# Kernel optimization log

Measured on AMD Instinct MI355X. Metric: run time of the kernel, lower is better.

The kernel has to match this reference:

```python
import jax, jax.numpy as jnp
import numpy as np

N_DENSE = 13
N_SPARSE = 26
EMBED_DIM = 16
VOCAB = 100000
N_PAIRS = N_SPARSE * (N_SPARSE - 1) // 2  # 325
I_IDX, J_IDX = np.triu_indices(N_SPARSE, k=1)  # loop order i<j matches tf code


def setup_inputs() -> dict:
    key = jax.random.key(0)
    ks = jax.random.split(key, 8)
    B = 2048
    inputs = jax.random.randint(ks[0], (B, N_DENSE + N_SPARSE), 0, VOCAB, dtype=jnp.int32)
    tables = jax.random.normal(ks[1], (N_SPARSE, VOCAB, EMBED_DIM), dtype=jnp.float32) * 0.05
    # Attention_layer: Dense(n_pairs, relu) applied along k, then Dense(1)
    w1 = jax.random.normal(ks[2], (EMBED_DIM, N_PAIRS), dtype=jnp.float32) * 0.05
    b1 = jnp.zeros((N_PAIRS,), dtype=jnp.float32)
    w2 = jax.random.normal(ks[3], (N_PAIRS, 1), dtype=jnp.float32) * 0.05
    b2 = jnp.zeros((1,), dtype=jnp.float32)
    wout = jax.random.normal(ks[4], (EMBED_DIM, 1), dtype=jnp.float32) * 0.05
    bout = jnp.zeros((1,), dtype=jnp.float32)
    return {"inputs": inputs, "tables": tables, "w1": w1, "b1": b1,
            "w2": w2, "b2": b2, "wout": wout, "bout": bout}


def reference(inputs, tables, w1, b1, w2, b2, wout, bout):
    sparse = inputs[:, N_DENSE:]                                  # [B, 26]
    # multi-table embedding lookup: tables[f, sparse[:, f]] for each field
    embed = tables[jnp.arange(N_SPARSE)[None, :], sparse]         # [B, 26, 16]
    # pairwise element-wise products (upper triangle, i<j)
    pairs = embed[:, I_IDX] * embed[:, J_IDX]                     # [B, 325, 16]
    # attention MLP (note: softmax over last axis of size 1 -> all ones, as in tf code)
    x = jax.nn.relu(pairs @ w1 + b1)                              # [B, 325, 325]
    score = x @ w2 + b2                                           # [B, 325, 1]
    a = jax.nn.softmax(score, axis=-1)                            # [B, 325, 1] (ones)
    pooled = jnp.matmul(jnp.swapaxes(a, 1, 2), pairs)             # [B, 1, 16]
    pooled = pooled.reshape(-1, EMBED_DIM)                        # [B, 16]
    return jax.nn.sigmoid(pooled @ wout + bout)                   # [B, 1]
```

## Files before the change

### kernel.cpp

```cpp
#include <hip/hip_runtime.h>
#include <math.h>

#define N_DENSE   13
#define N_SPARSE  26
#define EMBED_DIM 16
#define VOCAB     100000
#define NB        2048
#define NCOL      (N_DENSE + N_SPARSE)

__global__ __launch_bounds__(256) void afm_kernel(
    const int*   __restrict__ inputs,
    const float* __restrict__ tables,
    const float* __restrict__ wout,
    const float* __restrict__ bout,
    float*       __restrict__ out)
{
    int tid = blockIdx.x * blockDim.x + threadIdx.x;
    int b    = tid >> 5;
    int t    = tid & 31;
    int e    = t & 15;
    int half = t >> 4;
    if (b >= NB) return;

    const int* idx = inputs + b * NCOL + N_DENSE;

    float sum = 0.f, sumsq = 0.f;
    #pragma unroll
    for (int k = 0; k < 13; ++k) {
        int f = half * 13 + k;
        int ix = idx[f];
        float v = tables[((size_t)f * VOCAB + (size_t)ix) * EMBED_DIM + e];
        sum   += v;
        sumsq += v * v;
    }

    sum   += __shfl_xor(sum,   16, 32);
    sumsq += __shfl_xor(sumsq, 16, 32);

    float pooled  = 0.5f * (sum * sum - sumsq);
    float partial = pooled * wout[e];

    #pragma unroll
    for (int off = 8; off >= 1; off >>= 1)
        partial += __shfl_xor(partial, off, 16);

    if (t == 0) {
        float s = partial + bout[0];
        out[b] = 1.0f / (1.0f + expf(-s));
    }
}

extern "C" void kernel_launch(void* const* d_in, const int* in_sizes, int n_in,
                              void* d_out, int out_size, void* d_ws, size_t ws_size,
                              hipStream_t stream) {
    const int*   inputs = (const int*)  d_in[0];
    const float* tables = (const float*)d_in[1];
    const float* wout   = (const float*)d_in[6];
    const float* bout   = (const float*)d_in[7];
    float* out = (float*)d_out;

    const int threads_per_sample = 32;
    const int block = 256;
    const int total = NB * threads_per_sample;
    const int grid  = (total + block - 1) / block;

    afm_kernel<<<grid, block, 0, stream>>>(inputs, tables, wout, bout, out);
}
```

Before: 9.588 us.

## Use float4 embedding loads with 16 threads per sample and 4 field groups

Remaps the per-sample work so that each of 16 threads loads a float4 slice of an embedding row, with the 26 fields split across four groups. Sum and sum-of-squares reductions now cross groups via shuffles, and the output dot product reduces over 4 lanes. This cuts the thread count in half and issues 16-byte vector loads instead of scalar ones, which is meant to reduce instruction and memory-request overhead on the latency-bound gather. The cost is fewer threads to hide latency and a per-thread loop with a divergent tail for groups of 6 fields.

```diff
diff --git a/kernel.cpp b/kernel.cpp
--- a/kernel.cpp
+++ b/kernel.cpp
@@ -15,38 +15,50 @@
     const float* __restrict__ bout,
     float*       __restrict__ out)
 {
-    int tid = blockIdx.x * blockDim.x + threadIdx.x;
-    int b    = tid >> 5;
-    int t    = tid & 31;
-    int e    = t & 15;
-    int half = t >> 4;
+    int tid  = blockIdx.x * blockDim.x + threadIdx.x;
+    int b    = tid >> 4;
+    int t    = tid & 15;
+    int dim4 = t & 3;
+    int g    = t >> 2;
     if (b >= NB) return;
 
     const int* idx = inputs + b * NCOL + N_DENSE;
+    int start = (g < 2) ? 7 * g : 14 + 6 * (g - 2);
+    int cnt   = (g < 2) ? 7 : 6;
 
-    float sum = 0.f, sumsq = 0.f;
+    float s0 = 0.f, s1 = 0.f, s2 = 0.f, s3 = 0.f;
+    float q0 = 0.f, q1 = 0.f, q2 = 0.f, q3 = 0.f;
+
     #pragma unroll
-    for (int k = 0; k < 13; ++k) {
-        int f = half * 13 + k;
-        int ix = idx[f];
-        float v = tables[((size_t)f * VOCAB + (size_t)ix) * EMBED_DIM + e];
-        sum   += v;
-        sumsq += v * v;
+    for (int k = 0; k < 7; ++k) {
+        if (k < cnt) {
+            int f  = start + k;
+            int ix = idx[f];
+            const float4 v = *reinterpret_cast<const float4*>(
+                tables + ((size_t)f * VOCAB + (size_t)ix) * EMBED_DIM + dim4 * 4);
+            s0 += v.x; s1 += v.y; s2 += v.z; s3 += v.w;
+            q0 += v.x * v.x; q1 += v.y * v.y; q2 += v.z * v.z; q3 += v.w * v.w;
+        }
     }
 
-    sum   += __shfl_xor(sum,   16, 32);
-    sumsq += __shfl_xor(sumsq, 16, 32);
+    #pragma unroll
+    for (int off = 4; off <= 8; off <<= 1) {
+        s0 += __shfl_xor(s0, off, 16); s1 += __shfl_xor(s1, off, 16);
+        s2 += __shfl_xor(s2, off, 16); s3 += __shfl_xor(s3, off, 16);
+        q0 += __shfl_xor(q0, off, 16); q1 += __shfl_xor(q1, off, 16);
+        q2 += __shfl_xor(q2, off, 16); q3 += __shfl_xor(q3, off, 16);
+    }
 
-    float pooled  = 0.5f * (sum * sum - sumsq);
-    float partial = pooled * wout[e];
+    const float4 w = reinterpret_cast<const float4*>(wout)[dim4];
+    float partial = 0.5f * ((s0 * s0 - q0) * w.x + (s1 * s1 - q1) * w.y +
+                            (s2 * s2 - q2) * w.z + (s3 * s3 - q3) * w.w);
 
-    #pragma unroll
-    for (int off = 8; off >= 1; off >>= 1)
-        partial += __shfl_xor(partial, off, 16);
+    partial += __shfl_xor(partial, 1, 16);
+    partial += __shfl_xor(partial, 2, 16);
 
     if (t == 0) {
-        float s = partial + bout[0];
-        out[b] = 1.0f / (1.0f + expf(-s));
+        float sc = partial + bout[0];
+        out[b] = 1.0f / (1.0f + expf(-sc));
     }
 }
 
@@ -59,7 +71,7 @@
     const float* bout   = (const float*)d_in[7];
     float* out = (float*)d_out;
 
-    const int threads_per_sample = 32;
+    const int threads_per_sample = 16;
     const int block = 256;
     const int total = NB * threads_per_sample;
     const int grid  = (total + block - 1) / block;
```

Result: no change. 9.714 us (+1.3%).
